# Kernel optimization log

Hardware: AMD Instinct MI355X
Metric: run time of the kernel (lower is better)

Reference implementation:

```python
import jax, jax.numpy as jnp
import numpy as np

M, K, N = 32, 8192, 8192  # tokens, in_features, out_features
PACK = 8  # int4 nibbles per int32


def setup_inputs() -> dict:
    key = jax.random.key(0)
    k1, k2, k3, k4 = jax.random.split(key, 4)
    x = (jax.random.normal(k1, (M, K), dtype=jnp.float32)).astype(jnp.float16)
    # packed int4 weights: 8 signed nibbles per int32, [N, K//8]
    b_packed = jax.random.randint(k2, (N, K // PACK), 0, 2147483647, dtype=jnp.int32)
    # rowwise fp16 scales (meta), one per output row; small positive values
    scales = (jax.random.uniform(k3, (N,), dtype=jnp.float32) * 0.01 + 1e-4).astype(jnp.float16)
    bias = (jax.random.normal(k4, (N,), dtype=jnp.float32) * 0.01).astype(jnp.float16)
    return {"x": x, "b_packed": b_packed, "scales": scales, "bias": bias}


def _unpack_int4(b_packed):
    # b_packed: [N, K//8] int32 -> signed int4 values in [-8, 7], shape [N, K]
    shifts = (jnp.arange(PACK, dtype=jnp.int32) * 4)  # [8]
    nib = (b_packed[:, :, None] >> shifts) & 0xF       # [N, K//8, 8]
    q = jnp.where(nib >= 8, nib - 16, nib)             # two's-complement nibble
    return q.reshape(b_packed.shape[0], -1)            # [N, K]


def reference(x, b_packed, scales, bias):
    # Rowwise dequant: W[n, k] = q[n, k] * scale[n]  (fp16), then y = x @ W^T + bias
    q = _unpack_int4(b_packed).astype(jnp.float16)          # [N, K]
    W = q * scales[:, None]                                  # [N, K] fp16
    y = jnp.einsum('mk,nk->mn', x, W,
                   preferred_element_type=jnp.float32).astype(jnp.float16)
    y = y + bias.astype(y.dtype)
    return y
```

## Files before the change

kernel.cpp:

```cpp
#include <hip/hip_runtime.h>
#include <cstdint>

#define M_DIM 32
#define K_DIM 8192
#define N_DIM 8192

typedef _Float16 f16x8 __attribute__((ext_vector_type(8)));
typedef _Float16 f16x2 __attribute__((ext_vector_type(2)));
typedef float    f32x4 __attribute__((ext_vector_type(4)));

__device__ __forceinline__ uint32_t u4e(uint4 v, int t) {
  return (t == 0) ? v.x : (t == 1) ? v.y : (t == 2) ? v.z : v.w;
}

__device__ __forceinline__ f16x8 dq8(uint32_t w) {
  union { uint32_t u[4]; f16x8 v; } r;
  const uint32_t MASK  = 0x000F000Fu;
  const uint32_t MAGIC = 0x64086408u;
  const f16x2 magic = __builtin_bit_cast(f16x2, MAGIC);
#pragma unroll
  for (int s = 0; s < 4; ++s) {
    uint32_t t = ((w >> (4 * s)) & MASK) ^ MAGIC;
    f16x2 h = __builtin_bit_cast(f16x2, t) - magic;
    r.u[s] = __builtin_bit_cast(uint32_t, h);
  }
  return r.v;
}

__global__ __launch_bounds__(256) void xprep_kernel(
    const float* __restrict__ x, uint4* __restrict__ xp) {
  const int T = blockIdx.x * 256 + threadIdx.x;
  const int m = T >> 10;
  const int g = T & 1023;
  const f32x4* p = (const f32x4*)(x + (size_t)m * K_DIM + (size_t)g * 8);
  f32x4 lo = p[0], hi = p[1];
  union { uint4 q; f16x8 v; } o;
#pragma unroll
  for (int s = 0; s < 4; ++s) {
    o.v[2 * s]     = (_Float16)lo[s];
    o.v[2 * s + 1] = (_Float16)hi[s];
  }
  xp[(size_t)g * 32 + m] = o.q;
}

__global__ __launch_bounds__(1024, 8) void qgemm_xp16(
    const uint32_t* __restrict__ bq,
    const uint4*    __restrict__ xp,
    const float*    __restrict__ sc,
    const float*    __restrict__ bi,
    float*          __restrict__ out) {
  __shared__ float red[16][16][34];

  const int tid  = threadIdx.x;
  const int w    = tid >> 6;
  const int lane = tid & 63;
  const int l16  = lane & 15;
  const int quad = lane >> 4;
  const int n0   = blockIdx.x << 4;

  const uint4* bq4 = (const uint4*)bq;
  const uint4* bp0 = bq4 + (size_t)(n0 + l16) * 256 + (w << 4) + quad;
  const uint4* ap  = xp + (size_t)(((w << 6) + (quad << 2)) * 32 + l16);

  uint4 b0[4];
#pragma unroll
  for (int c = 0; c < 4; ++c) b0[c] = bp0[c * 4];

  f32x4 acc0 = {0.f, 0.f, 0.f, 0.f};
  f32x4 acc1 = {0.f, 0.f, 0.f, 0.f};

#pragma unroll
  for (int g = 0; g < 16; ++g) {
    const int c   = g >> 2, t = g & 3;
    const int off = (c * 16 + t) * 32;
    uint4 a0 = ap[off];
    uint4 a1 = ap[off + 16];
    f16x8 fb  = dq8(u4e(b0[c], t));
    f16x8 fa0 = __builtin_bit_cast(f16x8, a0);
    f16x8 fa1 = __builtin_bit_cast(f16x8, a1);
    acc0 = __builtin_amdgcn_mfma_f32_16x16x32_f16(fa0, fb, acc0, 0, 0, 0);
    acc1 = __builtin_amdgcn_mfma_f32_16x16x32_f16(fa1, fb, acc1, 0, 0, 0);
  }

#pragma unroll
  for (int r = 0; r < 4; ++r) {
    const int mr = (quad << 2) + r;
    red[w][l16][mr]      = acc0[r];
    red[w][l16][mr + 16] = acc1[r];
  }

  __syncthreads();

  if (tid < 512) {
    const int n = tid & 15;
    const int m = tid >> 4;
    float s = 0.f;
#pragma unroll
    for (int ww = 0; ww < 16; ++ww) s += red[ww][n][m];
    const int gn = n0 + n;
    out[(size_t)m * N_DIM + gn] = fmaf(s, sc[gn], bi[gn]);
  }
}

__global__ __launch_bounds__(512) void qgemm_direct(
    const uint32_t* __restrict__ bq, const float* __restrict__ x,
    const float* __restrict__ sc, const float* __restrict__ bi,
    float* __restrict__ out) {
  __shared__ float red[8][32][40];
  const int tid  = threadIdx.x;
  const int w    = tid >> 6;
  const int lane = tid & 63;
  const int l16  = lane & 15;
  const int quad = lane >> 4;
  const int n0   = blockIdx.x << 5;

  const uint4* bq4 = (const uint4*)bq;
  const uint4* bp0 = bq4 + (size_t)(n0 + l16) * 256 + (w << 5) + quad;
  const uint4* bp1 = bp0 + (size_t)16 * 256;
  const float* ap0 = x + (size_t)l16 * K_DIM + (w << 10) + (quad << 5);
  const float* ap1 = ap0 + (size_t)16 * K_DIM;

  f32x4 acc00 = {0.f,0.f,0.f,0.f}, acc01 = {0.f,0.f,0.f,0.f};
  f32x4 acc10 = {0.f,0.f,0.f,0.f}, acc11 = {0.f,0.f,0.f,0.f};
#pragma unroll
  for (int c = 0; c < 8; ++c) {
    const uint4 wb0 = bp0[c * 4];
    const uint4 wb1 = bp1[c * 4];
#pragma unroll
    for (int t = 0; t < 4; ++t) {
      const float* a0 = ap0 + c * 128 + t * 8;
      const float* a1 = ap1 + c * 128 + t * 8;
      f32x4 l0 = *(const f32x4*)a0, h0 = *(const f32x4*)(a0 + 4);
      f32x4 l1 = *(const f32x4*)a1, h1 = *(const f32x4*)(a1 + 4);
      f16x8 fa0, fa1;
#pragma unroll
      for (int s = 0; s < 4; ++s) {
        fa0[2*s] = (_Float16)l0[s]; fa0[2*s+1] = (_Float16)h0[s];
        fa1[2*s] = (_Float16)l1[s]; fa1[2*s+1] = (_Float16)h1[s];
      }
      f16x8 fb0 = dq8(u4e(wb0, t));
      f16x8 fb1 = dq8(u4e(wb1, t));
      acc00 = __builtin_amdgcn_mfma_f32_16x16x32_f16(fa0, fb0, acc00, 0, 0, 0);
      acc01 = __builtin_amdgcn_mfma_f32_16x16x32_f16(fa1, fb0, acc01, 0, 0, 0);
      acc10 = __builtin_amdgcn_mfma_f32_16x16x32_f16(fa0, fb1, acc10, 0, 0, 0);
      acc11 = __builtin_amdgcn_mfma_f32_16x16x32_f16(fa1, fb1, acc11, 0, 0, 0);
    }
  }
#pragma unroll
  for (int r = 0; r < 4; ++r) {
    const int mr = (quad << 2) + r;
    red[w][l16][mr]           = acc00[r];
    red[w][l16][mr + 16]      = acc01[r];
    red[w][l16 + 16][mr]      = acc10[r];
    red[w][l16 + 16][mr + 16] = acc11[r];
  }
  __syncthreads();
  const int n  = tid & 31;
  const int mh = tid >> 5;
  float s0 = 0.f, s1 = 0.f;
#pragma unroll
  for (int ww = 0; ww < 8; ++ww) { s0 += red[ww][n][mh]; s1 += red[ww][n][mh+16]; }
  const int gn = n0 + n;
  out[(size_t)mh * N_DIM + gn]        = fmaf(s0, sc[gn], bi[gn]);
  out[(size_t)(mh + 16) * N_DIM + gn] = fmaf(s1, sc[gn], bi[gn]);
}

extern "C" void kernel_launch(void* const* d_in, const int* in_sizes, int n_in,
                              void* d_out, int out_size, void* d_ws, size_t ws_size,
                              hipStream_t stream) {
  const float*    x  = (const float*)d_in[0];
  const uint32_t* bq = (const uint32_t*)d_in[1];
  const float*    sc = (const float*)d_in[2];
  const float*    bi = (const float*)d_in[3];
  float*          y  = (float*)d_out;

  const size_t XP_BYTES = (size_t)M_DIM * K_DIM * 2;
  if (ws_size >= XP_BYTES) {
    uint4* xp = (uint4*)d_ws;
    xprep_kernel<<<128, 256, 0, stream>>>(x, xp);
    qgemm_xp16<<<N_DIM / 16, 1024, 0, stream>>>(bq, xp, sc, bi, y);
  } else {
    qgemm_direct<<<N_DIM / 32, 512, 0, stream>>>(bq, x, sc, bi, y);
  }
}
```

Before: 93.18 us.

## Split K across blocks with global partial sums and separate reduce kernel

Replaces the 512-block, 1024-thread GEMM that reduced all 16 K-slices in shared memory with 8192 smaller 256-thread blocks, each covering one K-slice of a 16-column tile. Each block writes its partial sums to a workspace buffer, and a new reduce kernel sums the 16 slices and applies scale and bias. This is meant to give finer work distribution and better occupancy. In exchange it writes and reads about 16 MB of partials through global memory, adds a third launch, and needs a larger workspace.

```diff
diff --git a/kernel.cpp b/kernel.cpp
--- a/kernel.cpp
+++ b/kernel.cpp
@@ -43,39 +43,34 @@
   xp[(size_t)g * 32 + m] = o.q;
 }
 
-__global__ __launch_bounds__(1024, 8) void qgemm_xp16(
+__global__ __launch_bounds__(256, 4) void qgemm_ks(
     const uint32_t* __restrict__ bq,
     const uint4*    __restrict__ xp,
-    const float*    __restrict__ sc,
-    const float*    __restrict__ bi,
-    float*          __restrict__ out) {
-  __shared__ float red[16][16][34];
+    float*          __restrict__ part) {
+  __shared__ float red[4][16][33];
 
   const int tid  = threadIdx.x;
   const int w    = tid >> 6;
   const int lane = tid & 63;
   const int l16  = lane & 15;
   const int quad = lane >> 4;
-  const int n0   = blockIdx.x << 4;
+  const int bx   = blockIdx.x;
+  const int ks   = bx & 15;
+  const int nt   = bx >> 4;
+  const int n0   = nt << 4;
 
   const uint4* bq4 = (const uint4*)bq;
-  const uint4* bp0 = bq4 + (size_t)(n0 + l16) * 256 + (w << 4) + quad;
-  const uint4* ap  = xp + (size_t)(((w << 6) + (quad << 2)) * 32 + l16);
-
-  uint4 b0[4];
-#pragma unroll
-  for (int c = 0; c < 4; ++c) b0[c] = bp0[c * 4];
+  const uint4 b = bq4[(size_t)(n0 + l16) * 256 + (ks << 4) + (w << 2) + quad];
+
+  const uint4* ap = xp + (size_t)(((ks << 6) + (w << 4) + (quad << 2)) * 32 + l16);
 
   f32x4 acc0 = {0.f, 0.f, 0.f, 0.f};
   f32x4 acc1 = {0.f, 0.f, 0.f, 0.f};
-
-#pragma unroll
-  for (int g = 0; g < 16; ++g) {
-    const int c   = g >> 2, t = g & 3;
-    const int off = (c * 16 + t) * 32;
-    uint4 a0 = ap[off];
-    uint4 a1 = ap[off + 16];
-    f16x8 fb  = dq8(u4e(b0[c], t));
+#pragma unroll
+  for (int t = 0; t < 4; ++t) {
+    const uint4 a0 = ap[t * 32];
+    const uint4 a1 = ap[t * 32 + 16];
+    f16x8 fb  = dq8(u4e(b, t));
     f16x8 fa0 = __builtin_bit_cast(f16x8, a0);
     f16x8 fa1 = __builtin_bit_cast(f16x8, a1);
     acc0 = __builtin_amdgcn_mfma_f32_16x16x32_f16(fa0, fb, acc0, 0, 0, 0);
@@ -91,15 +86,34 @@
 
   __syncthreads();
 
-  if (tid < 512) {
-    const int n = tid & 15;
-    const int m = tid >> 4;
-    float s = 0.f;
-#pragma unroll
-    for (int ww = 0; ww < 16; ++ww) s += red[ww][n][m];
-    const int gn = n0 + n;
-    out[(size_t)m * N_DIM + gn] = fmaf(s, sc[gn], bi[gn]);
-  }
+  const int n = tid & 15;
+  const int m = tid >> 4;
+  float s0 = 0.f, s1 = 0.f;
+#pragma unroll
+  for (int ww = 0; ww < 4; ++ww) { s0 += red[ww][n][m]; s1 += red[ww][n][m + 16]; }
+  const int gn = n0 + n;
+  part[((size_t)ks * 32 + m) * N_DIM + gn]      = s0;
+  part[((size_t)ks * 32 + m + 16) * N_DIM + gn] = s1;
+}
+
+__global__ __launch_bounds__(256) void reduce_ks(
+    const float* __restrict__ part,
+    const float* __restrict__ sc,
+    const float* __restrict__ bi,
+    float*       __restrict__ out) {
+  const int T  = blockIdx.x * 256 + threadIdx.x;
+  const int m  = T >> 11;
+  const int n4 = T & 2047;
+  const f32x4* p = (const f32x4*)part + (size_t)m * 2048 + n4;
+  f32x4 s = {0.f, 0.f, 0.f, 0.f};
+#pragma unroll
+  for (int ks = 0; ks < 16; ++ks) s += p[(size_t)ks * 32 * 2048];
+  const f32x4 s4 = ((const f32x4*)sc)[n4];
+  const f32x4 b4 = ((const f32x4*)bi)[n4];
+  f32x4 r;
+#pragma unroll
+  for (int i = 0; i < 4; ++i) r[i] = fmaf(s[i], s4[i], b4[i]);
+  ((f32x4*)out)[(size_t)m * 2048 + n4] = r;
 }
 
 __global__ __launch_bounds__(512) void qgemm_direct(
@@ -174,11 +188,14 @@
   const float*    bi = (const float*)d_in[3];
   float*          y  = (float*)d_out;
 
-  const size_t XP_BYTES = (size_t)M_DIM * K_DIM * 2;
-  if (ws_size >= XP_BYTES) {
-    uint4* xp = (uint4*)d_ws;
+  const size_t XP_PAD = (size_t)1 << 20;
+  const size_t PART_B = (size_t)16 * 32 * N_DIM * 4;
+  if (ws_size >= XP_PAD + PART_B) {
+    uint4* xp   = (uint4*)d_ws;
+    float* part = (float*)((char*)d_ws + XP_PAD);
     xprep_kernel<<<128, 256, 0, stream>>>(x, xp);
-    qgemm_xp16<<<N_DIM / 16, 1024, 0, stream>>>(bq, xp, sc, bi, y);
+    qgemm_ks<<<8192, 256, 0, stream>>>(bq, xp, part);
+    reduce_ks<<<256, 256, 0, stream>>>(part, sc, bi, y);
   } else {
     qgemm_direct<<<N_DIM / 32, 512, 0, stream>>>(bq, x, sc, bi, y);
   }
```

Measured after the change: 96.87 us. 4.0% more time.
